# Kernel tuning notes

Hardware: AMD Instinct MI355X
Metric: run time of the kernel (lower is better)

## Reference

```python
import jax, jax.numpy as jnp
import numpy as np

N = 100000          # nodes
E = 3200000         # edges (avg degree 32)
IN_DIM = 256
HIDDEN = 64
OUT_DIM = 2
K = 10
ALPHA = 0.1
AVG_DEG = 32.0


def setup_inputs() -> dict:
    key = jax.random.key(0)
    ks = jax.random.split(key, 7)
    x = jax.random.normal(ks[0], (N, IN_DIM), dtype=jnp.float32)
    W1 = jax.random.normal(ks[1], (HIDDEN, IN_DIM), dtype=jnp.float32) * (1.0 / np.sqrt(IN_DIM))
    b1 = jnp.zeros((HIDDEN,), dtype=jnp.float32)
    W2 = jax.random.normal(ks[2], (OUT_DIM, HIDDEN), dtype=jnp.float32) * (1.0 / np.sqrt(HIDDEN))
    b2 = jnp.zeros((OUT_DIM,), dtype=jnp.float32)
    edge_rows = jax.random.randint(ks[3], (E,), 0, N, dtype=jnp.int32)
    edge_cols = jax.random.randint(ks[4], (E,), 0, N, dtype=jnp.int32)
    # normalized-adjacency-like values: row sums ~ 0.5 so the K-step power
    # iteration stays stable (mimics D^-1 A normalization)
    edge_vals = jax.random.uniform(ks[5], (E,), dtype=jnp.float32) / AVG_DEG
    return {"x": x, "W1": W1, "b1": b1, "W2": W2, "b2": b2,
            "edge_rows": edge_rows, "edge_cols": edge_cols, "edge_vals": edge_vals}


def reference(x, W1, b1, W2, b2, edge_rows, edge_cols, edge_vals):
    # MLP encoder (dropout is identity at inference)
    h = jax.nn.relu(x @ W1.T + b1)              # [N, HIDDEN]
    Z = h @ W2.T + b2                            # [N, OUT_DIM]

    # APPNP propagation: H <- alpha*Z + (1-alpha) * S @ H, K times
    def step(H, _):
        msg = edge_vals[:, None] * H[edge_cols]  # gather along cols, [E, OUT_DIM]
        SH = jax.ops.segment_sum(msg, edge_rows, num_segments=N)  # scatter-add to rows
        return ALPHA * Z + (1.0 - ALPHA) * SH, None

    H, _ = jax.lax.scan(step, Z, None, length=K)
    return H
```

## Files before the change

### kernel.cpp

```cpp
#include <hip/hip_runtime.h>

#define IN_DIM 256
#define HID 64
#define K_ITERS 10
#define ALPHA 0.1f

constexpr int RPB      = 128;
constexpr int BCAP     = 4992;
constexpr int OVF_CAP  = 8192;
constexpr int MAXBUCK  = 1024;
constexpr int BUILD_BLOCKS = 256;

typedef __attribute__((ext_vector_type(8))) short short8v;
typedef __attribute__((ext_vector_type(4))) float float4v;

__device__ __forceinline__ unsigned short f32_bf16(float f) {
  unsigned u = __float_as_uint(f);
  u += 0x7FFFu + ((u >> 16) & 1u);
  return (unsigned short)(u >> 16);
}
__device__ __forceinline__ float bf16_f32(unsigned short h) {
  return __uint_as_float((unsigned)h << 16);
}

__global__ __launch_bounds__(256) void w1_frag(
    const float* __restrict__ W1, unsigned short* __restrict__ W1F)
{
  int idx = blockIdx.x * 256 + threadIdx.x;
  int i  = idx & 7;
  int ln = (idx >> 3) & 63;
  int ht = (idx >> 9) & 3;
  int ks = idx >> 11;
  int hid = ht * 16 + (ln & 15);
  int k   = ks * 32 + (ln >> 4) * 8 + i;
  float v = W1[hid * IN_DIM + k];
  unsigned short hi = f32_bf16(v);
  unsigned short lo = f32_bf16(v - bf16_f32(hi));
  W1F[idx]         = hi;
  W1F[16384 + idx] = lo;
}

__global__ __launch_bounds__(256) void mlp_mfma(
    const float* __restrict__ x, const unsigned short* __restrict__ W1F,
    const float* __restrict__ b1, const float* __restrict__ W2,
    const float* __restrict__ b2, float* __restrict__ Z, int n)
{
  const int tid  = threadIdx.x;
  const int w    = tid >> 6;
  const int lane = tid & 63;
  const int m    = lane & 15;
  const int kg   = lane >> 4;
  const int node = blockIdx.x * 64 + w * 16 + m;
  const bool valid = node < n;
  const float* xrow = x + (size_t)(valid ? node : 0) * IN_DIM;

  const short8v* Bhi = reinterpret_cast<const short8v*>(W1F);
  const short8v* Blo = Bhi + 2048;

  float4v acc[4];
  #pragma unroll
  for (int ht = 0; ht < 4; ++ht) acc[ht] = (float4v){0.f, 0.f, 0.f, 0.f};

  #pragma unroll
  for (int ks = 0; ks < 8; ++ks) {
    const int kb = ks * 32 + kg * 8;
    float4 a0 = *reinterpret_cast<const float4*>(xrow + kb);
    float4 a1 = *reinterpret_cast<const float4*>(xrow + kb + 4);
    float xv[8] = {a0.x, a0.y, a0.z, a0.w, a1.x, a1.y, a1.z, a1.w};
    short8v ahi, alo;
    #pragma unroll
    for (int i = 0; i < 8; ++i) {
      unsigned short h = f32_bf16(xv[i]);
      ahi[i] = (short)h;
      alo[i] = (short)f32_bf16(xv[i] - bf16_f32(h));
    }
    #pragma unroll
    for (int ht = 0; ht < 4; ++ht) {
      int bidx = (ks * 4 + ht) * 64 + lane;
      short8v bh = Bhi[bidx];
      short8v bl = Blo[bidx];
      acc[ht] = __builtin_amdgcn_mfma_f32_16x16x32_bf16(ahi, bh, acc[ht], 0, 0, 0);
      acc[ht] = __builtin_amdgcn_mfma_f32_16x16x32_bf16(alo, bh, acc[ht], 0, 0, 0);
      acc[ht] = __builtin_amdgcn_mfma_f32_16x16x32_bf16(ahi, bl, acc[ht], 0, 0, 0);
    }
  }

  float p0[4] = {0.f, 0.f, 0.f, 0.f}, p1[4] = {0.f, 0.f, 0.f, 0.f};
  #pragma unroll
  for (int ht = 0; ht < 4; ++ht) {
    int hid = ht * 16 + m;
    float w0 = W2[hid], w1v = W2[HID + hid], bb = b1[hid];
    #pragma unroll
    for (int j = 0; j < 4; ++j) {
      float h = fmaxf(acc[ht][j] + bb, 0.f);
      p0[j] = fmaf(h, w0, p0[j]);
      p1[j] = fmaf(h, w1v, p1[j]);
    }
  }
  #pragma unroll
  for (int j = 0; j < 4; ++j) {
    #pragma unroll
    for (int s = 1; s < 16; s <<= 1) {
      p0[j] += __shfl_xor(p0[j], s);
      p1[j] += __shfl_xor(p1[j], s);
    }
  }
  if (m == 0) {
    #pragma unroll
    for (int j = 0; j < 4; ++j) {
      int nd = blockIdx.x * 64 + w * 16 + kg * 4 + j;
      if (nd < n) {
        Z[(size_t)nd * 2 + 0] = p0[j] + b2[0];
        Z[(size_t)nd * 2 + 1] = p1[j] + b2[1];
      }
    }
  }
}

__global__ __launch_bounds__(512) void bucket_build(
    const int* __restrict__ rows, const int* __restrict__ cols,
    const float* __restrict__ vals, int* __restrict__ gcnt,
    int2* __restrict__ binned, int4* __restrict__ ovf, int* __restrict__ ovfN,
    int e, int nbuck)
{
  __shared__ int h1[MAXBUCK];
  __shared__ int h2[MAXBUCK];
  __shared__ int base[MAXBUCK];
  const int tid = threadIdx.x;
  const int chunk = (e + gridDim.x - 1) / gridDim.x;
  const int beg = blockIdx.x * chunk;
  const int end = min(beg + chunk, e);

  for (int b = tid; b < nbuck; b += 512) { h1[b] = 0; h2[b] = 0; }
  __syncthreads();

  for (int i = beg + tid; i < end; i += 512)
    atomicAdd(&h1[rows[i] >> 7], 1);
  __syncthreads();

  for (int b = tid; b < nbuck; b += 512) {
    int c = h1[b];
    base[b] = c ? atomicAdd(&gcnt[b], c) : 0;
  }
  __syncthreads();

  for (int i = beg + tid; i < end; i += 512) {
    int r = rows[i];
    int b = r >> 7;
    int rank = atomicAdd(&h2[b], 1);
    int pos  = base[b] + rank;
    int rc   = ((r & 127) << 17) | cols[i];
    int vb   = __float_as_int(vals[i]);
    if (pos < BCAP) {
      binned[(size_t)b * BCAP + pos] = make_int2(rc, vb);
    } else {
      int k = atomicAdd(ovfN, 1);
      if (k < OVF_CAP) ovf[k] = make_int4(b, rc, vb, 0);
    }
  }
}

__global__ __launch_bounds__(512) void bucket_sort(
    const int* __restrict__ gcnt, int2* __restrict__ binned,
    int* __restrict__ rowoff, int nbuck)
{
  __shared__ int2 buf[BCAP];
  __shared__ int hist[RPB];
  __shared__ int offs[RPB];
  __shared__ int cur[RPB];
  const int b = blockIdx.x, tid = threadIdx.x;
  const int cnt = min(gcnt[b], BCAP);
  int2* gp = binned + (size_t)b * BCAP;

  if (tid < RPB) hist[tid] = 0;
  __syncthreads();
  for (int i = tid; i < cnt; i += 512) {
    int2 e = gp[i];
    buf[i] = e;
    atomicAdd(&hist[e.x >> 17], 1);
  }
  __syncthreads();
  if (tid == 0) {
    int run = 0;
    for (int r = 0; r < RPB; ++r) { offs[r] = run; cur[r] = run; run += hist[r]; }
  }
  __syncthreads();
  if (tid < RPB) rowoff[b * RPB + tid] = offs[tid];
  for (int i = tid; i < cnt; i += 512) {
    int2 e = buf[i];
    int pos = atomicAdd(&cur[e.x >> 17], 1);
    gp[pos] = e;
  }
}

__global__ __launch_bounds__(256) void sorted_gather(
    const int* __restrict__ rowoff, const int* __restrict__ gcnt,
    const int2* __restrict__ binned, const float* __restrict__ Z,
    const float* __restrict__ Hin, float* __restrict__ Hout,
    const int4* __restrict__ ovf, const int* __restrict__ ovfN,
    float cB, int n)
{
  int g = blockIdx.x * 256 + threadIdx.x;
  int r = g >> 2, l = g & 3;
  if (r >= n) return;
  int b = r >> 7, rl = r & 127;
  int cntraw = gcnt[b];
  int cnt = min(cntraw, BCAP);
  int beg = rowoff[b * RPB + rl];
  int end = (rl == RPB - 1) ? cnt : rowoff[b * RPB + rl + 1];
  const int2* bp = binned + (size_t)b * BCAP;
  float sx = 0.f, sy = 0.f;
  for (int i = beg + l; i < end; i += 4) {
    int2 p = bp[i];
    int col = p.x & 0x1FFFF;
    float v = __int_as_float(p.y);
    float2 h = *reinterpret_cast<const float2*>(&Hin[(size_t)col * 2]);
    sx += v * h.x; sy += v * h.y;
  }
  if (cntraw > BCAP) {
    int mo = min(*ovfN, OVF_CAP);
    for (int j = l; j < mo; j += 4) {
      int4 o = ovf[j];
      if (o.x == b && (o.y >> 17) == rl) {
        int col = o.y & 0x1FFFF;
        float v = __int_as_float(o.z);
        float2 h = *reinterpret_cast<const float2*>(&Hin[(size_t)col * 2]);
        sx += v * h.x; sy += v * h.y;
      }
    }
  }
  sx += __shfl_xor(sx, 1); sy += __shfl_xor(sy, 1);
  sx += __shfl_xor(sx, 2); sy += __shfl_xor(sy, 2);
  if (l == 0) {
    float2 z = *reinterpret_cast<const float2*>(&Z[(size_t)r * 2]);
    reinterpret_cast<float2*>(Hout)[r] =
        make_float2(ALPHA * z.x + cB * sx, ALPHA * z.y + cB * sy);
  }
}

extern "C" void kernel_launch(void* const* d_in, const int* in_sizes, int n_in,
                              void* d_out, int out_size, void* d_ws, size_t ws_size,
                              hipStream_t stream) {
  const float* x     = (const float*)d_in[0];
  const float* W1    = (const float*)d_in[1];
  const float* b1    = (const float*)d_in[2];
  const float* W2    = (const float*)d_in[3];
  const float* b2    = (const float*)d_in[4];
  const int*   erows = (const int*)d_in[5];
  const int*   ecols = (const int*)d_in[6];
  const float* evals = (const float*)d_in[7];
  float* out = (float*)d_out;

  const int n = in_sizes[0] / IN_DIM;
  const int e = in_sizes[5];
  const int nbuck = (n + RPB - 1) / RPB;

  char* ws = (char*)d_ws;
  int2*  binned = (int2*)ws;            ws += (size_t)nbuck * BCAP * sizeof(int2);
  int4*  ovf    = (int4*)ws;            ws += (size_t)OVF_CAP * sizeof(int4);
  float* Z      = (float*)ws;           ws += (size_t)n * 2 * sizeof(float);
  float* Ha     = (float*)ws;           ws += (size_t)n * 2 * sizeof(float);
  float* Hb     = (float*)ws;           ws += (size_t)n * 2 * sizeof(float);
  unsigned short* W1F = (unsigned short*)ws;  ws += 2 * 16384 * sizeof(unsigned short);
  int*   rowoff = (int*)ws;             ws += (size_t)nbuck * RPB * sizeof(int);
  int*   gcnt   = (int*)ws;             ws += (size_t)nbuck * sizeof(int);
  int*   ovfN   = (int*)ws;             ws += 4 * sizeof(int);

  hipMemsetAsync(gcnt, 0, (size_t)nbuck * sizeof(int), stream);
  hipMemsetAsync(ovfN, 0, sizeof(int), stream);

  bucket_build<<<BUILD_BLOCKS, 512, 0, stream>>>(erows, ecols, evals, gcnt,
                                                 binned, ovf, ovfN, e, nbuck);
  bucket_sort<<<nbuck, 512, 0, stream>>>(gcnt, binned, rowoff, nbuck);

  w1_frag<<<64, 256, 0, stream>>>(W1, W1F);
  mlp_mfma<<<(n + 63) / 64, 256, 0, stream>>>(x, W1F, b1, W2, b2, Z, n);

  const float cB = 1.f - ALPHA;
  const int grid_g = (4 * n + 255) / 256;
  const float* hin = Z;
  for (int t = 0; t < K_ITERS; ++t) {
    float* hout = (t == K_ITERS - 1) ? out : ((t & 1) ? Hb : Ha);
    sorted_gather<<<grid_g, 256, 0, stream>>>(rowoff, gcnt, binned, Z, hin, hout,
                                              ovf, ovfN, cB, n);
    hin = hout;
  }
}
```

Measured before the change: 341.5 us.

## Stage bucketed edges in LDS per block before coalesced global scatter

The edge bucketing kernel now sorts each block's chunk of edges by bucket inside shared memory, using a histogram, a prefix scan and local atomics. It then writes them to the global bucket arrays in runs that are contiguous per bucket, instead of scattering each edge straight to a random global slot. The aim is to turn scattered 8-byte global writes into mostly contiguous runs and to size the grid by a fixed chunk. In exchange, each block uses a large LDS footprint (~128KB) that limits occupancy, and nbuck must stay at or below 800.

```diff
diff --git a/kernel.cpp b/kernel.cpp
--- a/kernel.cpp
+++ b/kernel.cpp
@@ -8,8 +8,8 @@
 constexpr int RPB      = 128;
 constexpr int BCAP     = 4992;
 constexpr int OVF_CAP  = 8192;
-constexpr int MAXBUCK  = 1024;
-constexpr int BUILD_BLOCKS = 256;
+constexpr int MAXBUCK  = 800;
+constexpr int CHUNK    = 12544;
 
 typedef __attribute__((ext_vector_type(8))) short short8v;
 typedef __attribute__((ext_vector_type(4))) float float4v;
@@ -117,45 +117,68 @@
   }
 }
 
-__global__ __launch_bounds__(512) void bucket_build(
+__global__ __launch_bounds__(512) void bucket_build2(
     const int* __restrict__ rows, const int* __restrict__ cols,
     const float* __restrict__ vals, int* __restrict__ gcnt,
     int2* __restrict__ binned, int4* __restrict__ ovf, int* __restrict__ ovfN,
     int e, int nbuck)
 {
+  __shared__ int2 buf[CHUNK];
+  __shared__ unsigned short sb[CHUNK];
   __shared__ int h1[MAXBUCK];
-  __shared__ int h2[MAXBUCK];
-  __shared__ int base[MAXBUCK];
+  __shared__ int scn[2][MAXBUCK];
+  __shared__ int lofs[MAXBUCK];
+  __shared__ int cur[MAXBUCK];
+  __shared__ int gbase[MAXBUCK];
+
   const int tid = threadIdx.x;
-  const int chunk = (e + gridDim.x - 1) / gridDim.x;
-  const int beg = blockIdx.x * chunk;
-  const int end = min(beg + chunk, e);
-
-  for (int b = tid; b < nbuck; b += 512) { h1[b] = 0; h2[b] = 0; }
+  const int beg = blockIdx.x * CHUNK;
+  const int end = min(beg + CHUNK, e);
+  const int cnt = end - beg;
+
+  for (int b = tid; b < nbuck; b += 512) h1[b] = 0;
   __syncthreads();
 
   for (int i = beg + tid; i < end; i += 512)
     atomicAdd(&h1[rows[i] >> 7], 1);
   __syncthreads();
 
+  int p = 0;
+  for (int b = tid; b < nbuck; b += 512) scn[0][b] = h1[b];
+  __syncthreads();
+  for (int off = 1; off < nbuck; off <<= 1) {
+    for (int b = tid; b < nbuck; b += 512)
+      scn[p ^ 1][b] = (b >= off) ? scn[p][b] + scn[p][b - off] : scn[p][b];
+    __syncthreads();
+    p ^= 1;
+  }
   for (int b = tid; b < nbuck; b += 512) {
-    int c = h1[b];
-    base[b] = c ? atomicAdd(&gcnt[b], c) : 0;
+    int ex = (b == 0) ? 0 : scn[p][b - 1];
+    lofs[b] = ex;
+    cur[b]  = ex;
   }
   __syncthreads();
 
   for (int i = beg + tid; i < end; i += 512) {
     int r = rows[i];
     int b = r >> 7;
-    int rank = atomicAdd(&h2[b], 1);
-    int pos  = base[b] + rank;
-    int rc   = ((r & 127) << 17) | cols[i];
-    int vb   = __float_as_int(vals[i]);
+    int pos = atomicAdd(&cur[b], 1);
+    buf[pos] = make_int2(((r & 127) << 17) | cols[i], __float_as_int(vals[i]));
+    sb[pos]  = (unsigned short)b;
+  }
+  for (int b = tid; b < nbuck; b += 512)
+    gbase[b] = h1[b] ? atomicAdd(&gcnt[b], h1[b]) : 0;
+  __syncthreads();
+
+  for (int i = tid; i < cnt; i += 512) {
+    int b = sb[i];
+    int pos = gbase[b] + (i - lofs[b]);
+    int2 ed = buf[i];
     if (pos < BCAP) {
-      binned[(size_t)b * BCAP + pos] = make_int2(rc, vb);
+      binned[(size_t)b * BCAP + pos] = ed;
     } else {
       int k = atomicAdd(ovfN, 1);
-      if (k < OVF_CAP) ovf[k] = make_int4(b, rc, vb, 0);
+      if (k < OVF_CAP) ovf[k] = make_int4(b, ed.x, ed.y, 0);
     }
   }
 }
@@ -269,8 +292,9 @@
   hipMemsetAsync(gcnt, 0, (size_t)nbuck * sizeof(int), stream);
   hipMemsetAsync(ovfN, 0, sizeof(int), stream);
 
-  bucket_build<<<BUILD_BLOCKS, 512, 0, stream>>>(erows, ecols, evals, gcnt,
-                                                 binned, ovf, ovfN, e, nbuck);
+  const int grid_b = (e + CHUNK - 1) / CHUNK;
+  bucket_build2<<<grid_b, 512, 0, stream>>>(erows, ecols, evals, gcnt,
+                                            binned, ovf, ovfN, e, nbuck);
   bucket_sort<<<nbuck, 512, 0, stream>>>(gcnt, binned, rowoff, nbuck);
 
   w1_frag<<<64, 256, 0, stream>>>(W1, W1F);
```

Result: no change. 334.9 us (-1.9%).
